# Optimization experiments

Hardware: AMD Instinct MI355X
Metric: run time of the kernel (lower is better)

The kernel has to match this reference:

```python
import jax, jax.numpy as jnp
import numpy as np

B, C, H, W = 8, 256, 64, 64
CI = 128  # inter_channels = in_channels // reduction

def _conv1x1(x, w, b):
    # x: [b, c, h, w], w: [o, c], b: [o]
    return jnp.einsum('bchw,oc->bohw', x, w) + b[None, :, None, None]

def setup_inputs() -> dict:
    key = jax.random.key(0)
    ks = jax.random.split(key, 5)
    s_in = 1.0 / np.sqrt(C)
    s_ci = 1.0 / np.sqrt(CI)
    return {
        'x': jax.random.normal(ks[0], (B, C, H, W), jnp.float32),
        'w_g': jax.random.normal(ks[1], (CI, C), jnp.float32) * s_in,
        'b_g': jnp.zeros((CI,), jnp.float32),
        'w_theta': jax.random.normal(ks[2], (CI, C), jnp.float32) * s_in,
        'b_theta': jnp.zeros((CI,), jnp.float32),
        'w_phi': jax.random.normal(ks[3], (CI, C), jnp.float32) * s_in,
        'b_phi': jnp.zeros((CI,), jnp.float32),
        'w_out': jax.random.normal(ks[4], (C, CI), jnp.float32) * s_ci,
        'b_out': jnp.zeros((C,), jnp.float32),
    }

def reference(x, w_g, b_g, w_theta, b_theta, w_phi, b_phi, w_out, b_out):
    n, c, h, w = x.shape
    N = h * w
    g_x = _conv1x1(x, w_g, b_g).reshape(n, CI, N).transpose(0, 2, 1)        # [b, N, ci]
    theta_x = _conv1x1(x, w_theta, b_theta).reshape(n, CI, N).transpose(0, 2, 1)  # [b, N, ci]
    phi_x = _conv1x1(x, w_phi, b_phi).reshape(n, CI, N)                     # [b, ci, N]
    pw = jnp.einsum('bnc,bcm->bnm', theta_x, phi_x)                         # [b, N, N]
    # Faithful to source: divides by ci**(-0.5) == multiplies by sqrt(ci)
    pw = pw / (jnp.asarray(CI, x.dtype) ** -0.5)
    pw = jax.nn.softmax(pw, axis=-1)
    y = jnp.einsum('bnm,bmc->bnc', pw, g_x)                                 # [b, N, ci]
    y = y.transpose(0, 2, 1).reshape(n, CI, h, w)
    return x + _conv1x1(y, w_out, b_out)
```

## Files before the change

### kernel.cpp

```cpp
#include <hip/hip_runtime.h>
#include <hip/hip_bf16.h>
#include <stdint.h>
#include <stddef.h>


typedef __bf16 bf16;
typedef __attribute__((ext_vector_type(8))) __bf16 bf16x8;
typedef __attribute__((ext_vector_type(4))) __bf16 bf16x4;
typedef __attribute__((ext_vector_type(4))) float  f32x4;
typedef __attribute__((ext_vector_type(4))) int    i32x4;

#define MFMA16(a, b, c) __builtin_amdgcn_mfma_f32_16x16x32_bf16((a), (b), (c), 0, 0, 0)

constexpr int NB  = 8;
constexpr int NC  = 256;
constexpr int NN  = 4096;
constexpr int NCI = 128;
constexpr size_t NEL = (size_t)NB * NN * NCI;

__global__ __launch_bounds__(256) void k_proj(
    const float* __restrict__ x,
    const float* __restrict__ wt, const float* __restrict__ bt,
    const float* __restrict__ wp, const float* __restrict__ bp,
    const float* __restrict__ wg, const float* __restrict__ bg,
    bf16* __restrict__ qh, bf16* __restrict__ ql,
    bf16* __restrict__ kh, bf16* __restrict__ kl,
    bf16* __restrict__ vv)
{
    const int nt  = blockIdx.x;
    const int pj  = blockIdx.y;
    const int b   = blockIdx.z;
    const int tid = threadIdx.x;
    const int wv  = tid >> 6;
    const int ln  = tid & 63;
    const int lg  = ln >> 4;
    const int lq  = ln & 15;

    const float* W;
    const float* bias;
    if (pj == 0)      { W = wt; bias = bt; }
    else if (pj == 1) { W = wp; bias = bp; }
    else              { W = wg; bias = bg; }
    const bool split = (pj != 2);

    __shared__ char lds[49152];
    char* Ah = lds;
    char* Al = lds + 8192;
    char* Wh = lds + 16384;
    char* Wl = lds + 32768;

    f32x4 acc[8];
#pragma unroll
    for (int j = 0; j < 8; ++j) acc[j] = f32x4{0.f, 0.f, 0.f, 0.f};

    const int n0 = nt * 64;

    for (int c0 = 0; c0 < NC; c0 += 64) {
        __syncthreads();
#pragma unroll
        for (int p = 0; p < 4; ++p) {
            int cc = p * 16 + (tid >> 4);
            int nn = (tid & 15) * 4;
            f32x4 xv = *(const f32x4*)(x + ((size_t)b * NC + (c0 + cc)) * NN + n0 + nn);
#pragma unroll
            for (int e = 0; e < 4; ++e) {
                float f = xv[e];
                bf16 h = (bf16)f;
                int row = nn + e;
                int off = (row * 128 + cc * 2) ^ ((row & 7) << 4);
                *(bf16*)(Ah + off) = h;
                *(bf16*)(Al + off) = (bf16)(f - (float)h);
            }
        }
#pragma unroll
        for (int p = 0; p < 8; ++p) {
            int i  = p * 16 + (tid >> 4);
            int c4 = (tid & 15) * 4;
            f32x4 w4 = *(const f32x4*)(W + (size_t)i * NC + c0 + c4);
            bf16x4 hv, lv;
#pragma unroll
            for (int e = 0; e < 4; ++e) {
                bf16 h = (bf16)w4[e];
                hv[e] = h;
                lv[e] = (bf16)(w4[e] - (float)h);
            }
            int off = (i * 128 + c4 * 2) ^ ((i & 7) << 4);
            *(bf16x4*)(Wh + off) = hv;
            if (split) *(bf16x4*)(Wl + off) = lv;
        }
        __syncthreads();
#pragma unroll
        for (int kk = 0; kk < 2; ++kk) {
            int row  = wv * 16 + lq;
            int koff = kk * 64 + lg * 16;
            int aoff = (row * 128 + koff) ^ ((row & 7) << 4);
            bf16x8 ah = *(const bf16x8*)(Ah + aoff);
            bf16x8 al = *(const bf16x8*)(Al + aoff);
#pragma unroll
            for (int j = 0; j < 8; ++j) {
                int ir   = j * 16 + lq;
                int woff = (ir * 128 + koff) ^ ((ir & 7) << 4);
                bf16x8 bh = *(const bf16x8*)(Wh + woff);
                acc[j] = MFMA16(ah, bh, acc[j]);
                if (split) {
                    bf16x8 bl = *(const bf16x8*)(Wl + woff);
                    acc[j] = MFMA16(ah, bl, acc[j]);
                    acc[j] = MFMA16(al, bh, acc[j]);
                }
            }
        }
    }

    if (pj == 2) {
        __syncthreads();
        char* T = lds;
#pragma unroll
        for (int j = 0; j < 8; ++j) {
            int i = j * 16 + lq;
            float bv = bias[i];
#pragma unroll
            for (int r = 0; r < 4; ++r) {
                int nl = wv * 16 + lg * 4 + r;
                int off = (i * 128 + nl * 2) ^ ((i & 7) << 4);
                *(bf16*)(T + off) = (bf16)(acc[j][r] + bv);
            }
        }
        __syncthreads();
#pragma unroll
        for (int p = 0; p < 4; ++p) {
            int i  = p * 32 + (tid >> 3);
            int sl = tid & 7;
            i32x4 t = *(const i32x4*)(T + ((i * 128 + sl * 16) ^ ((i & 7) << 4)));
            *(i32x4*)(vv + ((size_t)b * NCI + i) * NN + n0 + sl * 8) = t;
        }
    } else {
#pragma unroll
        for (int j = 0; j < 8; ++j) {
            int i = j * 16 + lq;
            float bv = bias[i];
#pragma unroll
            for (int r = 0; r < 4; ++r) {
                int q = n0 + wv * 16 + lg * 4 + r;
                size_t off = ((size_t)b * NN + q) * NCI + i;
                float val = acc[j][r] + bv;
                bf16 h = (bf16)val;
                bf16 l = (bf16)(val - (float)h);
                if (pj == 0) { qh[off] = h; ql[off] = l; }
                else         { kh[off] = h; kl[off] = l; }
            }
        }
    }
}

__global__ __launch_bounds__(256, 1) void k_attn(
    const bf16* __restrict__ qh, const bf16* __restrict__ ql,
    const bf16* __restrict__ kh, const bf16* __restrict__ kl,
    const bf16* __restrict__ vt, bf16* __restrict__ y)
{
    const int bid = blockIdx.x;
    const int b   = bid & 7;
    const int qt  = bid >> 3;
    const int tid = threadIdx.x;
    const int wv  = tid >> 6;
    const int ln  = tid & 63;
    const int lg  = ln >> 4;
    const int lq  = ln & 15;
    const int n0  = qt * 128;

    __shared__ __attribute__((aligned(16))) char lds[114688];
    char* P = lds + 98304 + wv * 4096;

    const int smm = tid >> 4;
    const int ssl = tid & 15;
    const int svd = tid >> 3;
    const int svl = tid & 7;

    bf16x8 qhf[2][4], qlf[2][4];
#pragma unroll
    for (int q2 = 0; q2 < 2; ++q2) {
        int qrow = n0 + wv * 32 + q2 * 16 + lq;
        const bf16* bh = qh + ((size_t)b * NN + qrow) * NCI;
        const bf16* bl = ql + ((size_t)b * NN + qrow) * NCI;
#pragma unroll
        for (int kk = 0; kk < 4; ++kk) {
            qhf[q2][kk] = *(const bf16x8*)(bh + kk * 32 + lg * 8);
            qlf[q2][kk] = *(const bf16x8*)(bl + kk * 32 + lg * 8);
        }
    }

    f32x4 o[2][8];
#pragma unroll
    for (int q2 = 0; q2 < 2; ++q2)
#pragma unroll
        for (int j = 0; j < 8; ++j) o[q2][j] = f32x4{0.f, 0.f, 0.f, 0.f};
    float mrun[2] = {-1e30f, -1e30f};
    float lrun[2] = {0.f, 0.f};
    const float scale = 11.313708498984761f;

    {
#pragma unroll
        for (int p = 0; p < 4; ++p) {
            int mm = p * 16 + smm;
            size_t g = ((size_t)b * NN + mm) * NCI + ssl * 8;
            i32x4 h = *(const i32x4*)(kh + g);
            i32x4 l = *(const i32x4*)(kl + g);
            int off = (mm * 256 + ssl * 16) ^ ((mm & 7) << 4);
            *(i32x4*)(lds + off) = h;
            *(i32x4*)(lds + 16384 + off) = l;
        }
#pragma unroll
        for (int p = 0; p < 4; ++p) {
            int d = p * 32 + svd;
            size_t g = ((size_t)b * NCI + d) * NN + svl * 8;
            i32x4 v = *(const i32x4*)(vt + g);
            int off = (d * 128 + svl * 16) ^ ((d & 7) << 4);
            *(i32x4*)(lds + 32768 + off) = v;
        }
    }
    __syncthreads();

    for (int t = 0; t < 64; ++t) {
        const int cur = t & 1;
        char* KH  = lds + cur * 49152;
        char* KL  = KH + 16384;
        char* VT  = KH + 32768;
        char* KHn = lds + (cur ^ 1) * 49152;
        char* KLn = KHn + 16384;
        char* VTn = KHn + 32768;
        const int m0n = (t + 1) * 64;
        const bool pre = (t < 63);

        i32x4 rkh[4], rkl[4];
        if (pre) {
#pragma unroll
            for (int p = 0; p < 4; ++p) {
                size_t g = ((size_t)b * NN + m0n + p * 16 + smm) * NCI + ssl * 8;
                rkh[p] = *(const i32x4*)(kh + g);
                rkl[p] = *(const i32x4*)(kl + g);
            }
        }

        f32x4 s[4][2];
        __builtin_amdgcn_s_setprio(1);
#pragma unroll
        for (int jm = 0; jm < 4; ++jm) {
            s[jm][0] = f32x4{0.f, 0.f, 0.f, 0.f};
            s[jm][1] = f32x4{0.f, 0.f, 0.f, 0.f};
            const int mrow = jm * 16 + lq;
            const int sw = (mrow & 7) << 4;
#pragma unroll
            for (int kk = 0; kk < 4; ++kk) {
                int aoff = (mrow * 256 + kk * 64 + lg * 16) ^ sw;
                bf16x8 ah = *(const bf16x8*)(KH + aoff);
                bf16x8 al = *(const bf16x8*)(KL + aoff);
                s[jm][0] = MFMA16(ah, qhf[0][kk], s[jm][0]);
                s[jm][1] = MFMA16(ah, qhf[1][kk], s[jm][1]);
                s[jm][0] = MFMA16(al, qhf[0][kk], s[jm][0]);
                s[jm][1] = MFMA16(al, qhf[1][kk], s[jm][1]);
                s[jm][0] = MFMA16(ah, qlf[0][kk], s[jm][0]);
                s[jm][1] = MFMA16(ah, qlf[1][kk], s[jm][1]);
            }
        }
        __builtin_amdgcn_s_setprio(0);

        i32x4 rv[4];
        if (pre) {
#pragma unroll
            for (int p = 0; p < 4; ++p) {
                int mm = p * 16 + smm;
                int off = (mm * 256 + ssl * 16) ^ ((mm & 7) << 4);
                *(i32x4*)(KHn + off) = rkh[p];
                *(i32x4*)(KLn + off) = rkl[p];
            }
#pragma unroll
            for (int p = 0; p < 4; ++p) {
                size_t g = ((size_t)b * NCI + p * 32 + svd) * NN + m0n + svl * 8;
                rv[p] = *(const i32x4*)(vt + g);
            }
        }

        float tm[2];
        tm[0] = s[0][0][0];
        tm[1] = s[0][1][0];
#pragma unroll
        for (int jm = 0; jm < 4; ++jm)
#pragma unroll
            for (int r = 0; r < 4; ++r) {
                tm[0] = fmaxf(tm[0], s[jm][0][r]);
                tm[1] = fmaxf(tm[1], s[jm][1][r]);
            }
#pragma unroll
        for (int q2 = 0; q2 < 2; ++q2) {
            tm[q2] = fmaxf(tm[q2], __shfl_xor(tm[q2], 16));
            tm[q2] = fmaxf(tm[q2], __shfl_xor(tm[q2], 32));
        }
        float alpha[2], psum[2];
#pragma unroll
        for (int q2 = 0; q2 < 2; ++q2) {
            float mnew = fmaxf(mrun[q2], tm[q2] * scale);
            alpha[q2] = __expf(mrun[q2] - mnew);
            mrun[q2] = mnew;
            psum[q2] = 0.f;
        }
#pragma unroll
        for (int jm = 0; jm < 4; ++jm)
#pragma unroll
            for (int q2 = 0; q2 < 2; ++q2) {
                bf16x4 pk;
#pragma unroll
                for (int r = 0; r < 4; ++r) {
                    float e = __expf(s[jm][q2][r] * scale - mrun[q2]);
                    psum[q2] += e;
                    pk[r] = (bf16)e;
                }
                int row = q2 * 16 + lq;
                int off = (row * 128 + (jm * 16 + lg * 4) * 2) ^ ((lq & 7) << 4);
                *(bf16x4*)(P + off) = pk;
            }
#pragma unroll
        for (int q2 = 0; q2 < 2; ++q2) {
            psum[q2] += __shfl_xor(psum[q2], 16);
            psum[q2] += __shfl_xor(psum[q2], 32);
            lrun[q2] = lrun[q2] * alpha[q2] + psum[q2];
        }

        float av0[4], av1[4];
#pragma unroll
        for (int r = 0; r < 4; ++r) {
            av0[r] = __shfl(alpha[0], lg * 4 + r);
            av1[r] = __shfl(alpha[1], lg * 4 + r);
        }
#pragma unroll
        for (int j = 0; j < 8; ++j)
#pragma unroll
            for (int r = 0; r < 4; ++r) {
                o[0][j][r] *= av0[r];
                o[1][j][r] *= av1[r];
            }

        bf16x8 pa[2][2];
#pragma unroll
        for (int q2 = 0; q2 < 2; ++q2)
#pragma unroll
            for (int tt = 0; tt < 2; ++tt) {
                int row = q2 * 16 + lq;
                pa[q2][tt] = *(const bf16x8*)(P + ((row * 128 + tt * 64 + lg * 16) ^ ((lq & 7) << 4)));
            }
        __builtin_amdgcn_s_setprio(1);
#pragma unroll
        for (int j = 0; j < 8; ++j) {
            int d = j * 16 + lq;
            int swv = (lq & 7) << 4;
#pragma unroll
            for (int tt = 0; tt < 2; ++tt) {
                bf16x8 bv = *(const bf16x8*)(VT + ((d * 128 + tt * 64 + lg * 16) ^ swv));
                o[0][j] = MFMA16(pa[0][tt], bv, o[0][j]);
                o[1][j] = MFMA16(pa[1][tt], bv, o[1][j]);
            }
        }
        __builtin_amdgcn_s_setprio(0);

        if (pre) {
#pragma unroll
            for (int p = 0; p < 4; ++p) {
                int d = p * 32 + svd;
                int off = (d * 128 + svl * 16) ^ ((d & 7) << 4);
                *(i32x4*)(VTn + off) = rv[p];
            }
        }
        __syncthreads();
    }

    float rl0[4], rl1[4];
#pragma unroll
    for (int r = 0; r < 4; ++r) {
        rl0[r] = 1.f / __shfl(lrun[0], lg * 4 + r);
        rl1[r] = 1.f / __shfl(lrun[1], lg * 4 + r);
    }
#pragma unroll
    for (int j = 0; j < 8; ++j) {
        int d = j * 16 + lq;
#pragma unroll
        for (int r = 0; r < 4; ++r) {
            int q0 = n0 + wv * 32 + lg * 4 + r;
            y[((size_t)b * NN + q0) * NCI + d]      = (bf16)(o[0][j][r] * rl0[r]);
            y[((size_t)b * NN + q0 + 16) * NCI + d] = (bf16)(o[1][j][r] * rl1[r]);
        }
    }
}

__global__ __launch_bounds__(256) void k_out(
    const bf16* __restrict__ y, const float* __restrict__ x,
    const float* __restrict__ w_out, const float* __restrict__ b_out,
    float* __restrict__ out)
{
    const int nt  = blockIdx.x;
    const int b   = blockIdx.y;
    const int tid = threadIdx.x;
    const int wv  = tid >> 6;
    const int ln  = tid & 63;
    const int lg  = ln >> 4;
    const int lq  = ln & 15;
    const int n0  = nt * 64;

    __shared__ char Y[16384];
#pragma unroll
    for (int p = 0; p < 4; ++p) {
        int nn = p * 16 + (tid >> 4);
        int d0 = (tid & 15) * 8;
        i32x4 t = *(const i32x4*)(y + ((size_t)b * NN + n0 + nn) * NCI + d0);
        *(i32x4*)(Y + ((nn * 256 + d0 * 2) ^ ((nn & 7) << 4))) = t;
    }
    __syncthreads();

    bf16x8 af[4];
    {
        int row = wv * 16 + lq;
#pragma unroll
        for (int kk = 0; kk < 4; ++kk) {
            int koff = kk * 64 + lg * 16;
            af[kk] = *(const bf16x8*)(Y + ((row * 256 + koff) ^ ((row & 7) << 4)));
        }
    }

    f32x4 acc[16];
#pragma unroll
    for (int j = 0; j < 16; ++j) acc[j] = f32x4{0.f, 0.f, 0.f, 0.f};

#pragma unroll
    for (int j = 0; j < 16; ++j) {
        int c = j * 16 + lq;
#pragma unroll
        for (int kk = 0; kk < 4; ++kk) {
            int i0 = kk * 32 + lg * 8;
            f32x4 wa = *(const f32x4*)(w_out + (size_t)c * NCI + i0);
            f32x4 wb = *(const f32x4*)(w_out + (size_t)c * NCI + i0 + 4);
            bf16x8 bw;
#pragma unroll
            for (int e = 0; e < 4; ++e) { bw[e] = (bf16)wa[e]; bw[e + 4] = (bf16)wb[e]; }
            acc[j] = MFMA16(af[kk], bw, acc[j]);
        }
    }

#pragma unroll
    for (int j = 0; j < 16; ++j) {
        int c = j * 16 + lq;
        int nb = n0 + wv * 16 + lg * 4;
        size_t off = ((size_t)b * NC + c) * (size_t)NN + nb;
        f32x4 xv = *(const f32x4*)(x + off);
        float bo = b_out[c];
        f32x4 r;
#pragma unroll
        for (int t = 0; t < 4; ++t) r[t] = acc[j][t] + xv[t] + bo;
        *(f32x4*)(out + off) = r;
    }
}

extern "C" void kernel_launch(void* const* d_in, const int* in_sizes, int n_in,
                              void* d_out, int out_size, void* d_ws, size_t ws_size,
                              hipStream_t stream)
{
    (void)in_sizes; (void)n_in; (void)out_size; (void)ws_size;
    const float* x  = (const float*)d_in[0];
    const float* wg = (const float*)d_in[1];
    const float* bg = (const float*)d_in[2];
    const float* wt = (const float*)d_in[3];
    const float* bt = (const float*)d_in[4];
    const float* wp = (const float*)d_in[5];
    const float* bp = (const float*)d_in[6];
    const float* wo = (const float*)d_in[7];
    const float* bo = (const float*)d_in[8];
    float* out = (float*)d_out;

    char* ws = (char*)d_ws;
    bf16* qh = (bf16*)(ws);
    bf16* ql = (bf16*)(ws + NEL * 2);
    bf16* kh = (bf16*)(ws + NEL * 4);
    bf16* kl = (bf16*)(ws + NEL * 6);
    bf16* vv = (bf16*)(ws + NEL * 8);
    bf16* y  = qh;

    k_proj<<<dim3(64, 3, 8), 256, 0, stream>>>(x, wt, bt, wp, bp, wg, bg,
                                               qh, ql, kh, kl, vv);
    k_attn<<<dim3(256), 256, 0, stream>>>(qh, ql, kh, kl, vv, y);
    k_out<<<dim3(64, 8), 256, 0, stream>>>(y, x, wo, bo, out);
}
```

Baseline: 278.6 us.

## Split attention over two key halves with a combine kernel

Adds a split-K flash-attention kernel that launches 512 blocks, each handling half of the key sequence. Each block writes normalized partial outputs together with its running max and sum, and a small combine kernel merges the two halves. The aim is to fill more compute units than the original 256-block launch, which is sized to the MI355X's 256 CUs. The new kernel also uses a smaller LDS footprint and allows two blocks per CU. In exchange it adds extra workspace traffic and one more launch, and it falls back to the old kernel when the workspace is too small.

```diff
diff --git a/kernel.cpp b/kernel.cpp
--- a/kernel.cpp
+++ b/kernel.cpp
@@ -152,7 +152,276 @@
     }
 }
 
-__global__ __launch_bounds__(256, 1) void k_attn(
+__global__ __launch_bounds__(256, 2) void k_attn_sp(
+    const bf16* __restrict__ qh, const bf16* __restrict__ ql,
+    const bf16* __restrict__ kh, const bf16* __restrict__ kl,
+    const bf16* __restrict__ vt,
+    bf16* __restrict__ p0, bf16* __restrict__ p1, float* __restrict__ ml)
+{
+    const int bid = blockIdx.x;
+    const int b   = bid & 7;
+    const int rs  = bid >> 3;
+    const int qt  = rs & 31;
+    const int h   = rs >> 5;
+    const int tid = threadIdx.x;
+    const int wv  = tid >> 6;
+    const int ln  = tid & 63;
+    const int lg  = ln >> 4;
+    const int lq  = ln & 15;
+    const int n0  = qt * 128;
+    const int mb0 = h * 2048;
+    bf16* ph = h ? p1 : p0;
+
+    __shared__ __attribute__((aligned(16))) char lds[65536];
+    char* KH = lds;
+    char* KL = lds + 16384;
+    char* VT = lds + 32768;
+    char* P  = lds + 49152 + wv * 4096;
+
+    const int smm = tid >> 4;
+    const int ssl = tid & 15;
+    const int svd = tid >> 3;
+    const int svl = tid & 7;
+
+    bf16x8 qhf[2][4], qlf[2][4];
+#pragma unroll
+    for (int q2 = 0; q2 < 2; ++q2) {
+        int qrow = n0 + wv * 32 + q2 * 16 + lq;
+        const bf16* bh = qh + ((size_t)b * NN + qrow) * NCI;
+        const bf16* bl = ql + ((size_t)b * NN + qrow) * NCI;
+#pragma unroll
+        for (int kk = 0; kk < 4; ++kk) {
+            qhf[q2][kk] = *(const bf16x8*)(bh + kk * 32 + lg * 8);
+            qlf[q2][kk] = *(const bf16x8*)(bl + kk * 32 + lg * 8);
+        }
+    }
+
+    f32x4 o[2][8];
+#pragma unroll
+    for (int q2 = 0; q2 < 2; ++q2)
+#pragma unroll
+        for (int j = 0; j < 8; ++j) o[q2][j] = f32x4{0.f, 0.f, 0.f, 0.f};
+    float mrun[2] = {-1e30f, -1e30f};
+    float lrun[2] = {0.f, 0.f};
+    const float scale = 11.313708498984761f;
+
+    {
+#pragma unroll
+        for (int p = 0; p < 4; ++p) {
+            int mm = p * 16 + smm;
+            size_t g = ((size_t)b * NN + mb0 + mm) * NCI + ssl * 8;
+            i32x4 hv = *(const i32x4*)(kh + g);
+            i32x4 lv = *(const i32x4*)(kl + g);
+            int off = (mm * 256 + ssl * 16) ^ ((mm & 7) << 4);
+            *(i32x4*)(KH + off) = hv;
+            *(i32x4*)(KL + off) = lv;
+        }
+#pragma unroll
+        for (int p = 0; p < 4; ++p) {
+            int d = p * 32 + svd;
+            size_t g = ((size_t)b * NCI + d) * NN + mb0 + svl * 8;
+            i32x4 v = *(const i32x4*)(vt + g);
+            int off = (d * 128 + svl * 16) ^ ((d & 7) << 4);
+            *(i32x4*)(VT + off) = v;
+        }
+    }
+    __syncthreads();
+
+    for (int t = 0; t < 32; ++t) {
+        const bool pre = (t < 31);
+        const int m0n = mb0 + (t + 1) * 64;
+
+        i32x4 rkh[4], rkl[4];
+        if (pre) {
+#pragma unroll
+            for (int p = 0; p < 4; ++p) {
+                size_t g = ((size_t)b * NN + m0n + p * 16 + smm) * NCI + ssl * 8;
+                rkh[p] = *(const i32x4*)(kh + g);
+                rkl[p] = *(const i32x4*)(kl + g);
+            }
+        }
+
+        f32x4 s[4][2];
+        __builtin_amdgcn_s_setprio(1);
+#pragma unroll
+        for (int jm = 0; jm < 4; ++jm) {
+            s[jm][0] = f32x4{0.f, 0.f, 0.f, 0.f};
+            s[jm][1] = f32x4{0.f, 0.f, 0.f, 0.f};
+            const int mrow = jm * 16 + lq;
+            const int sw = (mrow & 7) << 4;
+#pragma unroll
+            for (int kk = 0; kk < 4; ++kk) {
+                int aoff = (mrow * 256 + kk * 64 + lg * 16) ^ sw;
+                bf16x8 ah = *(const bf16x8*)(KH + aoff);
+                bf16x8 al = *(const bf16x8*)(KL + aoff);
+                s[jm][0] = MFMA16(ah, qhf[0][kk], s[jm][0]);
+                s[jm][1] = MFMA16(ah, qhf[1][kk], s[jm][1]);
+                s[jm][0] = MFMA16(al, qhf[0][kk], s[jm][0]);
+                s[jm][1] = MFMA16(al, qhf[1][kk], s[jm][1]);
+                s[jm][0] = MFMA16(ah, qlf[0][kk], s[jm][0]);
+                s[jm][1] = MFMA16(ah, qlf[1][kk], s[jm][1]);
+            }
+        }
+        __builtin_amdgcn_s_setprio(0);
+
+        i32x4 rv[4];
+        if (pre) {
+#pragma unroll
+            for (int p = 0; p < 4; ++p) {
+                size_t g = ((size_t)b * NCI + p * 32 + svd) * NN + m0n + svl * 8;
+                rv[p] = *(const i32x4*)(vt + g);
+            }
+        }
+
+        float tm[2];
+        tm[0] = s[0][0][0];
+        tm[1] = s[0][1][0];
+#pragma unroll
+        for (int jm = 0; jm < 4; ++jm)
+#pragma unroll
+            for (int r = 0; r < 4; ++r) {
+                tm[0] = fmaxf(tm[0], s[jm][0][r]);
+                tm[1] = fmaxf(tm[1], s[jm][1][r]);
+            }
+#pragma unroll
+        for (int q2 = 0; q2 < 2; ++q2) {
+            tm[q2] = fmaxf(tm[q2], __shfl_xor(tm[q2], 16));
+            tm[q2] = fmaxf(tm[q2], __shfl_xor(tm[q2], 32));
+        }
+        float alpha[2], psum[2];
+#pragma unroll
+        for (int q2 = 0; q2 < 2; ++q2) {
+            float mnew = fmaxf(mrun[q2], tm[q2] * scale);
+            alpha[q2] = __expf(mrun[q2] - mnew);
+            mrun[q2] = mnew;
+            psum[q2] = 0.f;
+        }
+#pragma unroll
+        for (int jm = 0; jm < 4; ++jm)
+#pragma unroll
+            for (int q2 = 0; q2 < 2; ++q2) {
+                bf16x4 pk;
+#pragma unroll
+                for (int r = 0; r < 4; ++r) {
+                    float e = __expf(s[jm][q2][r] * scale - mrun[q2]);
+                    psum[q2] += e;
+                    pk[r] = (bf16)e;
+                }
+                int row = q2 * 16 + lq;
+                int off = (row * 128 + (jm * 16 + lg * 4) * 2) ^ ((lq & 7) << 4);
+                *(bf16x4*)(P + off) = pk;
+            }
+#pragma unroll
+        for (int q2 = 0; q2 < 2; ++q2) {
+            psum[q2] += __shfl_xor(psum[q2], 16);
+            psum[q2] += __shfl_xor(psum[q2], 32);
+            lrun[q2] = lrun[q2] * alpha[q2] + psum[q2];
+        }
+
+        float av0[4], av1[4];
+#pragma unroll
+        for (int r = 0; r < 4; ++r) {
+            av0[r] = __shfl(alpha[0], lg * 4 + r);
+            av1[r] = __shfl(alpha[1], lg * 4 + r);
+        }
+#pragma unroll
+        for (int j = 0; j < 8; ++j)
+#pragma unroll
+            for (int r = 0; r < 4; ++r) {
+                o[0][j][r] *= av0[r];
+                o[1][j][r] *= av1[r];
+            }
+
+        bf16x8 pa[2][2];
+#pragma unroll
+        for (int q2 = 0; q2 < 2; ++q2)
+#pragma unroll
+            for (int tt = 0; tt < 2; ++tt) {
+                int row = q2 * 16 + lq;
+                pa[q2][tt] = *(const bf16x8*)(P + ((row * 128 + tt * 64 + lg * 16) ^ ((lq & 7) << 4)));
+            }
+        __builtin_amdgcn_s_setprio(1);
+#pragma unroll
+        for (int j = 0; j < 8; ++j) {
+            int d = j * 16 + lq;
+            int swv = (lq & 7) << 4;
+#pragma unroll
+            for (int tt = 0; tt < 2; ++tt) {
+                bf16x8 bv = *(const bf16x8*)(VT + ((d * 128 + tt * 64 + lg * 16) ^ swv));
+                o[0][j] = MFMA16(pa[0][tt], bv, o[0][j]);
+                o[1][j] = MFMA16(pa[1][tt], bv, o[1][j]);
+            }
+        }
+        __builtin_amdgcn_s_setprio(0);
+
+        if (pre) {
+            __syncthreads();
+#pragma unroll
+            for (int p = 0; p < 4; ++p) {
+                int mm = p * 16 + smm;
+                int off = (mm * 256 + ssl * 16) ^ ((mm & 7) << 4);
+                *(i32x4*)(KH + off) = rkh[p];
+                *(i32x4*)(KL + off) = rkl[p];
+            }
+#pragma unroll
+            for (int p = 0; p < 4; ++p) {
+                int d = p * 32 + svd;
+                int off = (d * 128 + svl * 16) ^ ((d & 7) << 4);
+                *(i32x4*)(VT + off) = rv[p];
+            }
+            __syncthreads();
+        }
+    }
+
+    float rl0[4], rl1[4];
+#pragma unroll
+    for (int r = 0; r < 4; ++r) {
+        rl0[r] = 1.f / __shfl(lrun[0], lg * 4 + r);
+        rl1[r] = 1.f / __shfl(lrun[1], lg * 4 + r);
+    }
+#pragma unroll
+    for (int j = 0; j < 8; ++j) {
+        int d = j * 16 + lq;
+#pragma unroll
+        for (int r = 0; r < 4; ++r) {
+            int q0 = n0 + wv * 32 + lg * 4 + r;
+            ph[((size_t)b * NN + q0) * NCI + d]      = (bf16)(o[0][j][r] * rl0[r]);
+            ph[((size_t)b * NN + q0 + 16) * NCI + d] = (bf16)(o[1][j][r] * rl1[r]);
+        }
+    }
+    if (lg == 0) {
+#pragma unroll
+        for (int q2 = 0; q2 < 2; ++q2) {
+            int row = n0 + wv * 32 + q2 * 16 + lq;
+            size_t base = ((size_t)b * NN + row) * 4 + h * 2;
+            ml[base]     = mrun[q2];
+            ml[base + 1] = lrun[q2];
+        }
+    }
+}
+
+__global__ __launch_bounds__(256) void k_comb(
+    const bf16* __restrict__ p0, const bf16* __restrict__ p1,
+    const float* __restrict__ ml, bf16* __restrict__ y)
+{
+    int row = blockIdx.x * 16 + (threadIdx.x >> 4);
+    int d0  = (threadIdx.x & 15) * 8;
+    f32x4 q = *(const f32x4*)(ml + (size_t)row * 4);
+    float M  = fmaxf(q[0], q[2]);
+    float w0 = __expf(q[0] - M) * q[1];
+    float w1 = __expf(q[2] - M) * q[3];
+    float inv = 1.f / (w0 + w1);
+    w0 *= inv; w1 *= inv;
+    size_t off = (size_t)row * NCI + d0;
+    bf16x8 a = *(const bf16x8*)(p0 + off);
+    bf16x8 c = *(const bf16x8*)(p1 + off);
+    bf16x8 r;
+#pragma unroll
+    for (int e = 0; e < 8; ++e) r[e] = (bf16)(w0 * (float)a[e] + w1 * (float)c[e]);
+    *(bf16x8*)(y + off) = r;
+}
+
+__global__ __launch_bounds__(256, 1) void k_attn_ns(
     const bf16* __restrict__ qh, const bf16* __restrict__ ql,
     const bf16* __restrict__ kh, const bf16* __restrict__ kl,
     const bf16* __restrict__ vt, bf16* __restrict__ y)
@@ -460,7 +729,7 @@
                               void* d_out, int out_size, void* d_ws, size_t ws_size,
                               hipStream_t stream)
 {
-    (void)in_sizes; (void)n_in; (void)out_size; (void)ws_size;
+    (void)in_sizes; (void)n_in; (void)out_size;
     const float* x  = (const float*)d_in[0];
     const float* wg = (const float*)d_in[1];
     const float* bg = (const float*)d_in[2];
@@ -479,9 +748,18 @@
     bf16* kl = (bf16*)(ws + NEL * 6);
     bf16* vv = (bf16*)(ws + NEL * 8);
     bf16* y  = qh;
+    bf16* p0 = (bf16*)(ws + NEL * 10);
+    bf16* p1 = (bf16*)(ws + NEL * 12);
+    float* ml = (float*)(ws + NEL * 14);
+    const size_t need = NEL * 14 + (size_t)NB * NN * 4 * sizeof(float);
 
     k_proj<<<dim3(64, 3, 8), 256, 0, stream>>>(x, wt, bt, wp, bp, wg, bg,
                                                qh, ql, kh, kl, vv);
-    k_attn<<<dim3(256), 256, 0, stream>>>(qh, ql, kh, kl, vv, y);
+    if (ws_size >= need) {
+        k_attn_sp<<<dim3(512), 256, 0, stream>>>(qh, ql, kh, kl, vv, p0, p1, ml);
+        k_comb<<<dim3(2048), 256, 0, stream>>>(p0, p1, ml, y);
+    } else {
+        k_attn_ns<<<dim3(256), 256, 0, stream>>>(qh, ql, kh, kl, vv, y);
+    }
     k_out<<<dim3(64, 8), 256, 0, stream>>>(y, x, wo, bo, out);
 }
```

After: 291.1 us. 1.04x slower.

## Split attention over key halves, load K/V directly from global, lazy rescale

Applied to the files above, without the earlier changes.

Splits the key dimension in two so the attention kernel launches twice as many blocks, then adds a combine kernel that merges the two partial softmax outputs using the saved running max and sum. The K/V LDS staging and double buffering are removed, so MFMA operands are read straight from global memory (L2), which shrinks LDS and allows two blocks per CU. The softmax scale and log2(e) are folded into Q in the projection kernel so exp2f is used, and rescaling of the output accumulators is skipped unless the running max grows by more than 8. In exchange it adds extra global traffic for the partial outputs, an extra kernel launch, and uncached, uncoalesced-pattern global loads inside the inner loop.

```diff
diff --git a/kernel.cpp b/kernel.cpp
--- a/kernel.cpp
+++ b/kernel.cpp
@@ -17,6 +17,8 @@
 constexpr int NN  = 4096;
 constexpr int NCI = 128;
 constexpr size_t NEL = (size_t)NB * NN * NCI;
+
+#define QSCALE (11.313708498984761f * 1.4426950408889634f)
 
 __global__ __launch_bounds__(256) void k_proj(
     const float* __restrict__ x,
@@ -134,6 +136,7 @@
             *(i32x4*)(vv + ((size_t)b * NCI + i) * NN + n0 + sl * 8) = t;
         }
     } else {
+        const float sc = (pj == 0) ? QSCALE : 1.0f;
 #pragma unroll
         for (int j = 0; j < 8; ++j) {
             int i = j * 16 + lq;
@@ -142,7 +145,7 @@
             for (int r = 0; r < 4; ++r) {
                 int q = n0 + wv * 16 + lg * 4 + r;
                 size_t off = ((size_t)b * NN + q) * NCI + i;
-                float val = acc[j][r] + bv;
+                float val = (acc[j][r] + bv) * sc;
                 bf16 h = (bf16)val;
                 bf16 l = (bf16)(val - (float)h);
                 if (pj == 0) { qh[off] = h; ql[off] = l; }
@@ -152,28 +155,28 @@
     }
 }
 
-__global__ __launch_bounds__(256, 1) void k_attn(
+__global__ __launch_bounds__(256, 2) void k_attn_sp(
     const bf16* __restrict__ qh, const bf16* __restrict__ ql,
     const bf16* __restrict__ kh, const bf16* __restrict__ kl,
-    const bf16* __restrict__ vt, bf16* __restrict__ y)
+    const bf16* __restrict__ vt,
+    bf16* __restrict__ p0, bf16* __restrict__ p1, float* __restrict__ ml)
 {
     const int bid = blockIdx.x;
     const int b   = bid & 7;
-    const int qt  = bid >> 3;
+    const int rs  = bid >> 3;
+    const int qt  = rs & 31;
+    const int h   = rs >> 5;
     const int tid = threadIdx.x;
     const int wv  = tid >> 6;
     const int ln  = tid & 63;
     const int lg  = ln >> 4;
     const int lq  = ln & 15;
     const int n0  = qt * 128;
-
-    __shared__ __attribute__((aligned(16))) char lds[114688];
-    char* P = lds + 98304 + wv * 4096;
-
-    const int smm = tid >> 4;
-    const int ssl = tid & 15;
-    const int svd = tid >> 3;
-    const int svl = tid & 7;
+    const int mb0 = h * 2048;
+    bf16* ph = h ? p1 : p0;
+
+    __shared__ __attribute__((aligned(16))) char lds[16384];
+    char* P = lds + wv * 4096;
 
     bf16x8 qhf[2][4], qlf[2][4];
 #pragma unroll
@@ -195,89 +198,39 @@
         for (int j = 0; j < 8; ++j) o[q2][j] = f32x4{0.f, 0.f, 0.f, 0.f};
     float mrun[2] = {-1e30f, -1e30f};
     float lrun[2] = {0.f, 0.f};
-    const float scale = 11.313708498984761f;
-
-    {
-#pragma unroll
-        for (int p = 0; p < 4; ++p) {
-            int mm = p * 16 + smm;
-            size_t g = ((size_t)b * NN + mm) * NCI + ssl * 8;
-            i32x4 h = *(const i32x4*)(kh + g);
-            i32x4 l = *(const i32x4*)(kl + g);
-            int off = (mm * 256 + ssl * 16) ^ ((mm & 7) << 4);
-            *(i32x4*)(lds + off) = h;
-            *(i32x4*)(lds + 16384 + off) = l;
-        }
-#pragma unroll
-        for (int p = 0; p < 4; ++p) {
-            int d = p * 32 + svd;
-            size_t g = ((size_t)b * NCI + d) * NN + svl * 8;
-            i32x4 v = *(const i32x4*)(vt + g);
-            int off = (d * 128 + svl * 16) ^ ((d & 7) << 4);
-            *(i32x4*)(lds + 32768 + off) = v;
-        }
-    }
-    __syncthreads();
-
-    for (int t = 0; t < 64; ++t) {
-        const int cur = t & 1;
-        char* KH  = lds + cur * 49152;
-        char* KL  = KH + 16384;
-        char* VT  = KH + 32768;
-        char* KHn = lds + (cur ^ 1) * 49152;
-        char* KLn = KHn + 16384;
-        char* VTn = KHn + 32768;
-        const int m0n = (t + 1) * 64;
-        const bool pre = (t < 63);
-
-        i32x4 rkh[4], rkl[4];
-        if (pre) {
-#pragma unroll
-            for (int p = 0; p < 4; ++p) {
-                size_t g = ((size_t)b * NN + m0n + p * 16 + smm) * NCI + ssl * 8;
-                rkh[p] = *(const i32x4*)(kh + g);
-                rkl[p] = *(const i32x4*)(kl + g);
-            }
-        }
+
+    const size_t krow0 = ((size_t)b * NN + mb0 + lq) * NCI + lg * 8;
+    const bf16* vbase  = vt + ((size_t)b * NCI + lq) * NN + mb0 + lg * 8;
+
+    for (int t = 0; t < 32; ++t) {
+        const int m0l = t * 64;
 
         f32x4 s[4][2];
         __builtin_amdgcn_s_setprio(1);
 #pragma unroll
         for (int jm = 0; jm < 4; ++jm) {
+            const size_t ro = krow0 + (size_t)(m0l + jm * 16) * NCI;
+            const bf16* kr = kh + ro;
+            const bf16* lr = kl + ro;
+            bf16x8 ah[4], al[4];
+#pragma unroll
+            for (int kk = 0; kk < 4; ++kk) {
+                ah[kk] = *(const bf16x8*)(kr + kk * 32);
+                al[kk] = *(const bf16x8*)(lr + kk * 32);
+            }
             s[jm][0] = f32x4{0.f, 0.f, 0.f, 0.f};
             s[jm][1] = f32x4{0.f, 0.f, 0.f, 0.f};
-            const int mrow = jm * 16 + lq;
-            const int sw = (mrow & 7) << 4;
 #pragma unroll
             for (int kk = 0; kk < 4; ++kk) {
-                int aoff = (mrow * 256 + kk * 64 + lg * 16) ^ sw;
-                bf16x8 ah = *(const bf16x8*)(KH + aoff);
-                bf16x8 al = *(const bf16x8*)(KL + aoff);
-                s[jm][0] = MFMA16(ah, qhf[0][kk], s[jm][0]);
-                s[jm][1] = MFMA16(ah, qhf[1][kk], s[jm][1]);
-                s[jm][0] = MFMA16(al, qhf[0][kk], s[jm][0]);
-                s[jm][1] = MFMA16(al, qhf[1][kk], s[jm][1]);
-                s[jm][0] = MFMA16(ah, qlf[0][kk], s[jm][0]);
-                s[jm][1] = MFMA16(ah, qlf[1][kk], s[jm][1]);
+                s[jm][0] = MFMA16(ah[kk], qhf[0][kk], s[jm][0]);
+                s[jm][1] = MFMA16(ah[kk], qhf[1][kk], s[jm][1]);
+                s[jm][0] = MFMA16(al[kk], qhf[0][kk], s[jm][0]);
+                s[jm][1] = MFMA16(al[kk], qhf[1][kk], s[jm][1]);
+                s[jm][0] = MFMA16(ah[kk], qlf[0][kk], s[jm][0]);
+                s[jm][1] = MFMA16(ah[kk], qlf[1][kk], s[jm][1]);
             }
         }
         __builtin_amdgcn_s_setprio(0);
-
-        i32x4 rv[4];
-        if (pre) {
-#pragma unroll
-            for (int p = 0; p < 4; ++p) {
-                int mm = p * 16 + smm;
-                int off = (mm * 256 + ssl * 16) ^ ((mm & 7) << 4);
-                *(i32x4*)(KHn + off) = rkh[p];
-                *(i32x4*)(KLn + off) = rkl[p];
-            }
-#pragma unroll
-            for (int p = 0; p < 4; ++p) {
-                size_t g = ((size_t)b * NCI + p * 32 + svd) * NN + m0n + svl * 8;
-                rv[p] = *(const i32x4*)(vt + g);
-            }
-        }
 
         float tm[2];
         tm[0] = s[0][0][0];
@@ -294,14 +247,33 @@
             tm[q2] = fmaxf(tm[q2], __shfl_xor(tm[q2], 16));
             tm[q2] = fmaxf(tm[q2], __shfl_xor(tm[q2], 32));
         }
-        float alpha[2], psum[2];
-#pragma unroll
-        for (int q2 = 0; q2 < 2; ++q2) {
-            float mnew = fmaxf(mrun[q2], tm[q2] * scale);
-            alpha[q2] = __expf(mrun[q2] - mnew);
-            mrun[q2] = mnew;
-            psum[q2] = 0.f;
-        }
+
+        bool grow = (tm[0] > mrun[0] + 8.f) || (tm[1] > mrun[1] + 8.f);
+        if (__any(grow)) {
+            float alpha[2];
+#pragma unroll
+            for (int q2 = 0; q2 < 2; ++q2) {
+                float mnew = fmaxf(mrun[q2], tm[q2]);
+                alpha[q2] = exp2f(mrun[q2] - mnew);
+                mrun[q2] = mnew;
+                lrun[q2] *= alpha[q2];
+            }
+            float av0[4], av1[4];
+#pragma unroll
+            for (int r = 0; r < 4; ++r) {
+                av0[r] = __shfl(alpha[0], lg * 4 + r);
+                av1[r] = __shfl(alpha[1], lg * 4 + r);
+            }
+#pragma unroll
+            for (int j = 0; j < 8; ++j)
+#pragma unroll
+                for (int r = 0; r < 4; ++r) {
+                    o[0][j][r] *= av0[r];
+                    o[1][j][r] *= av1[r];
+                }
+        }
+
+        float psum[2] = {0.f, 0.f};
 #pragma unroll
         for (int jm = 0; jm < 4; ++jm)
 #pragma unroll
@@ -309,7 +281,7 @@
                 bf16x4 pk;
 #pragma unroll
                 for (int r = 0; r < 4; ++r) {
-                    float e = __expf(s[jm][q2][r] * scale - mrun[q2]);
+                    float e = exp2f(s[jm][q2][r] - mrun[q2]);
                     psum[q2] += e;
                     pk[r] = (bf16)e;
                 }
@@ -321,22 +293,8 @@
         for (int q2 = 0; q2 < 2; ++q2) {
             psum[q2] += __shfl_xor(psum[q2], 16);
             psum[q2] += __shfl_xor(psum[q2], 32);
-            lrun[q2] = lrun[q2] * alpha[q2] + psum[q2];
-        }
-
-        float av0[4], av1[4];
-#pragma unroll
-        for (int r = 0; r < 4; ++r) {
-            av0[r] = __shfl(alpha[0], lg * 4 + r);
-            av1[r] = __shfl(alpha[1], lg * 4 + r);
-        }
-#pragma unroll
-        for (int j = 0; j < 8; ++j)
-#pragma unroll
-            for (int r = 0; r < 4; ++r) {
-                o[0][j][r] *= av0[r];
-                o[1][j][r] *= av1[r];
-            }
+            lrun[q2] += psum[q2];
+        }
 
         bf16x8 pa[2][2];
 #pragma unroll
@@ -349,26 +307,15 @@
         __builtin_amdgcn_s_setprio(1);
 #pragma unroll
         for (int j = 0; j < 8; ++j) {
-            int d = j * 16 + lq;
-            int swv = (lq & 7) << 4;
-#pragma unroll
-            for (int tt = 0; tt < 2; ++tt) {
-                bf16x8 bv = *(const bf16x8*)(VT + ((d * 128 + tt * 64 + lg * 16) ^ swv));
-                o[0][j] = MFMA16(pa[0][tt], bv, o[0][j]);
-                o[1][j] = MFMA16(pa[1][tt], bv, o[1][j]);
-            }
+            const bf16* vr = vbase + (size_t)(j * 16) * NN + m0l;
+            bf16x8 bv0 = *(const bf16x8*)(vr);
+            bf16x8 bv1 = *(const bf16x8*)(vr + 32);
+            o[0][j] = MFMA16(pa[0][0], bv0, o[0][j]);
+            o[1][j] = MFMA16(pa[1][0], bv0, o[1][j]);
+            o[0][j] = MFMA16(pa[0][1], bv1, o[0][j]);
+            o[1][j] = MFMA16(pa[1][1], bv1, o[1][j]);
         }
         __builtin_amdgcn_s_setprio(0);
-
-        if (pre) {
-#pragma unroll
-            for (int p = 0; p < 4; ++p) {
-                int d = p * 32 + svd;
-                int off = (d * 128 + svl * 16) ^ ((d & 7) << 4);
-                *(i32x4*)(VTn + off) = rv[p];
-            }
-        }
-        __syncthreads();
     }
 
     float rl0[4], rl1[4];
@@ -383,10 +330,40 @@
 #pragma unroll
         for (int r = 0; r < 4; ++r) {
             int q0 = n0 + wv * 32 + lg * 4 + r;
-            y[((size_t)b * NN + q0) * NCI + d]      = (bf16)(o[0][j][r] * rl0[r]);
-            y[((size_t)b * NN + q0 + 16) * NCI + d] = (bf16)(o[1][j][r] * rl1[r]);
-        }
-    }
+            ph[((size_t)b * NN + q0) * NCI + d]      = (bf16)(o[0][j][r] * rl0[r]);
+            ph[((size_t)b * NN + q0 + 16) * NCI + d] = (bf16)(o[1][j][r] * rl1[r]);
+        }
+    }
+    if (lg == 0) {
+#pragma unroll
+        for (int q2 = 0; q2 < 2; ++q2) {
+            int row = n0 + wv * 32 + q2 * 16 + lq;
+            size_t base = ((size_t)b * NN + row) * 4 + h * 2;
+            ml[base]     = mrun[q2];
+            ml[base + 1] = lrun[q2];
+        }
+    }
+}
+
+__global__ __launch_bounds__(256) void k_comb(
+    const bf16* __restrict__ p0, const bf16* __restrict__ p1,
+    const float* __restrict__ ml, bf16* __restrict__ y)
+{
+    int row = blockIdx.x * 16 + (threadIdx.x >> 4);
+    int d0  = (threadIdx.x & 15) * 8;
+    f32x4 q = *(const f32x4*)(ml + (size_t)row * 4);
+    float M  = fmaxf(q[0], q[2]);
+    float w0 = exp2f(q[0] - M) * q[1];
+    float w1 = exp2f(q[2] - M) * q[3];
+    float inv = 1.f / (w0 + w1);
+    w0 *= inv; w1 *= inv;
+    size_t off = (size_t)row * NCI + d0;
+    bf16x8 a = *(const bf16x8*)(p0 + off);
+    bf16x8 c = *(const bf16x8*)(p1 + off);
+    bf16x8 r;
+#pragma unroll
+    for (int e = 0; e < 8; ++e) r[e] = (bf16)(w0 * (float)a[e] + w1 * (float)c[e]);
+    *(bf16x8*)(y + off) = r;
 }
 
 __global__ __launch_bounds__(256) void k_out(
@@ -479,9 +456,13 @@
     bf16* kl = (bf16*)(ws + NEL * 6);
     bf16* vv = (bf16*)(ws + NEL * 8);
     bf16* y  = qh;
+    bf16* p0 = (bf16*)(ws + NEL * 10);
+    bf16* p1 = (bf16*)(ws + NEL * 12);
+    float* ml = (float*)(ws + NEL * 14);
 
     k_proj<<<dim3(64, 3, 8), 256, 0, stream>>>(x, wt, bt, wp, bp, wg, bg,
                                                qh, ql, kh, kl, vv);
-    k_attn<<<dim3(256), 256, 0, stream>>>(qh, ql, kh, kl, vv, y);
+    k_attn_sp<<<dim3(512), 256, 0, stream>>>(qh, ql, kh, kl, vv, p0, p1, ml);
+    k_comb<<<dim3(2048), 256, 0, stream>>>(p0, p1, ml, y);
     k_out<<<dim3(64, 8), 256, 0, stream>>>(y, x, wo, bo, out);
 }
```

New measurement: 443.5 us. +59.2%, slower.
